# Optimization experiments

Hardware: AMD Instinct MI355X
Metric: run time of the kernel (lower is better)

## Reference

```python
import jax, jax.numpy as jnp
import numpy as np

N = 100000
E = 1600000
D_IN = 128
H1 = 128
H2 = 128
C = 64


def setup_inputs() -> dict:
    key = jax.random.key(0)
    ks = jax.random.split(key, 10)
    x_content = jax.random.normal(ks[0], (N, D_IN), dtype=jnp.float32)
    edge_index = jax.random.randint(ks[1], (2, E), 0, N, dtype=jnp.int64)
    # SAGEConv params: lin_l (applied to aggregated neighbors, has bias),
    # lin_r (applied to root node, no bias). Kaiming-ish scaling.
    def lin(k, fan_in, fan_out):
        return jax.random.normal(k, (fan_in, fan_out), dtype=jnp.float32) / np.sqrt(fan_in)
    return {
        "x_content": x_content,
        "edge_index": edge_index,
        "W1l": lin(ks[2], D_IN, H1),
        "b1": jnp.zeros((H1,), jnp.float32),
        "W1r": lin(ks[3], D_IN, H1),
        "W2l": lin(ks[4], H1, H2),
        "b2": jnp.zeros((H2,), jnp.float32),
        "W2r": lin(ks[5], H1, H2),
        "Wout": lin(ks[6], H2, C),
        "bout": jnp.zeros((C,), jnp.float32),
    }


def _sage_conv(x, src, dst, Wl, b, Wr):
    # mean-aggregate neighbor features (messages flow src -> dst), then
    # out = mean_agg @ Wl + b + x @ Wr  (PyG SAGEConv, aggr='mean')
    msgs = x[src]                                            # [E, d]
    agg = jax.ops.segment_sum(msgs, dst, num_segments=N)     # [N, d]
    deg = jax.ops.segment_sum(jnp.ones((src.shape[0],), x.dtype), dst, num_segments=N)
    mean = agg / jnp.clip(deg, 1.0)[:, None]
    return mean @ Wl + b + x @ Wr


def reference(x_content, edge_index, W1l, b1, W1r, W2l, b2, W2r, Wout, bout):
    src, dst = edge_index[0], edge_index[1]
    # dropout is identity in eval mode (training=False)
    x = jax.nn.relu(_sage_conv(x_content, src, dst, W1l, b1, W1r))
    x = jax.nn.relu(_sage_conv(x, src, dst, W2l, b2, W2r))
    return x @ Wout + bout
```

## Files before the change

### kernel.cpp

```cpp
#include <hip/hip_runtime.h>
#include <hip/hip_fp8.h>

#define DD 128
#define CC 64
#define BKW 512
#define NPB 4096
#define CAP 10240

typedef __attribute__((ext_vector_type(8))) short short8v;
typedef __attribute__((ext_vector_type(4))) float f32x4;
typedef __attribute__((ext_vector_type(2))) float f32x2;

static __device__ inline ushort f2bf_rne(float f) {
    unsigned u = __float_as_uint(f);
    unsigned r = (u + 0x7FFFu + ((u >> 16) & 1u)) >> 16;
    return (ushort)r;
}
static __device__ inline float bf2f(ushort h) {
    return __uint_as_float(((unsigned)h) << 16);
}

__global__ void binit_kernel(int* __restrict__ bcur, int nbuck) {
    int b = blockIdx.x * 256 + threadIdx.x;
    if (b < nbuck) bcur[b] = b * CAP;
}

__global__ __launch_bounds__(256) void binA_kernel(const int* __restrict__ ei,
                                                   int* __restrict__ bcur,
                                                   uint* __restrict__ ebuf, int E) {
    __shared__ int sRun[256];
    __shared__ int sRel[256];
    __shared__ int sBase[256];
    __shared__ uint sPair[NPB];
    __shared__ unsigned char sBkt[NPB];
    __shared__ int sHist[256];
    const int t = threadIdx.x;
    const int e0 = blockIdx.x * NPB;
    const int cntE = min(NPB, E - e0);

    sHist[t] = 0;
    __syncthreads();
    for (int j = t; j < cntE; j += 256) {
        int dst = ei[E + e0 + j];
        atomicAdd(&sHist[dst >> 9], 1);
    }
    __syncthreads();
    int h = sHist[t];
    sRun[t] = h;
    __syncthreads();
    for (int off = 1; off < 256; off <<= 1) {
        int v = 0;
        if (t >= off) v = sRun[t - off];
        __syncthreads();
        if (t >= off) sRun[t] += v;
        __syncthreads();
    }
    int runstart = sRun[t] - h;
    int base = 0;
    if (h > 0) base = atomicAdd(&bcur[t], h);
    sRun[t] = runstart;
    sRel[t] = runstart;
    sBase[t] = base;
    __syncthreads();
    for (int j = t; j < cntE; j += 256) {
        int src = ei[e0 + j];
        int dst = ei[E + e0 + j];
        int b = dst >> 9;
        int slot = atomicAdd(&sRel[b], 1);
        sPair[slot] = (uint)src | ((uint)(dst & 511) << 17);
        sBkt[slot] = (unsigned char)b;
    }
    __syncthreads();
    for (int s = t; s < cntE; s += 256) {
        uint p = sPair[s];
        int b = (int)sBkt[s];
        int gpos = sBase[b] + (s - sRun[b]);
        ebuf[gpos] = p;
    }
}

__global__ __launch_bounds__(256) void binB2_kernel(const uint* __restrict__ ebuf,
                                                    const int* __restrict__ bcur,
                                                    int* __restrict__ offs,
                                                    int* __restrict__ cnt,
                                                    int* __restrict__ csr, int n) {
    __shared__ int sCnt[BKW];
    __shared__ int sOffs[BKW];
    __shared__ int sScan[256];
    const int t = threadIdx.x;
    const int node0 = blockIdx.x * BKW;
    const int start = blockIdx.x * CAP;
    const int end = bcur[blockIdx.x];

    sCnt[t] = 0; sCnt[t + 256] = 0;
    __syncthreads();
    for (int j = start + t; j < end; j += 256) {
        int d = (int)(ebuf[j] >> 17);
        atomicAdd(&sCnt[d], 1);
    }
    __syncthreads();
    int v0 = sCnt[2 * t], v1 = sCnt[2 * t + 1];
    int sum = v0 + v1;
    sScan[t] = sum;
    __syncthreads();
    for (int off = 1; off < 256; off <<= 1) {
        int xv = 0;
        if (t >= off) xv = sScan[t - off];
        __syncthreads();
        if (t >= off) sScan[t] += xv;
        __syncthreads();
    }
    int excl = sScan[t] - sum;
    sOffs[2 * t] = start + excl;
    sOffs[2 * t + 1] = start + excl + v0;
    __syncthreads();
    for (int i = t; i < BKW; i += 256) {
        int node = node0 + i;
        if (node < n) { offs[node] = sOffs[i]; cnt[node] = sCnt[i]; }
    }
    __syncthreads();
    sCnt[t] = 0; sCnt[t + 256] = 0;
    __syncthreads();
    for (int j = start + t; j < end; j += 256) {
        uint p = ebuf[j];
        int d = (int)(p >> 17);
        int r = atomicAdd(&sCnt[d], 1);
        csr[sOffs[d] + r] = (int)(p & 0x1FFFFu);
    }
}

__global__ __launch_bounds__(256) void prep_kernel(
    const float* __restrict__ x, ushort* __restrict__ xh, uint* __restrict__ xq,
    const float* __restrict__ Wl1, const float* __restrict__ Wr1,
    const float* __restrict__ Wl2, const float* __restrict__ Wr2,
    const float* __restrict__ Wout,
    ushort* __restrict__ WTfrag1, ushort* __restrict__ WTfrag2,
    ushort* __restrict__ WoFrag, int nxblk) {
    const int t = threadIdx.x;
    const int bx = blockIdx.x;
    if (bx < nxblk) {
        int i = bx * 256 + t;
        float4 a = ((const float4*)x)[2 * i];
        float4 b = ((const float4*)x)[2 * i + 1];
        float vv[8] = {a.x, a.y, a.z, a.w, b.x, b.y, b.z, b.w};
        ushort r[8];
        uint q[8];
        #pragma unroll
        for (int j = 0; j < 8; ++j) {
            r[j] = f2bf_rne(vv[j]);
            q[j] = (uint)__hip_fp8_e4m3(vv[j]).__x;
        }
        uint4 o;
        o.x = (uint)r[0] | ((uint)r[1] << 16);
        o.y = (uint)r[2] | ((uint)r[3] << 16);
        o.z = (uint)r[4] | ((uint)r[5] << 16);
        o.w = (uint)r[6] | ((uint)r[7] << 16);
        ((uint4*)xh)[i] = o;
        uint2 oq;
        oq.x = q[0] | (q[1] << 8) | (q[2] << 16) | (q[3] << 24);
        oq.y = q[4] | (q[5] << 8) | (q[6] << 16) | (q[7] << 24);
        ((uint2*)xq)[i] = oq;
    } else if (bx < nxblk + 32) {
        int li = bx - nxblk;
        int layer = li >> 4;
        int idx = (li & 15) * 256 + t;
        const float* Wl = layer ? Wl2 : Wl1;
        const float* Wr = layer ? Wr2 : Wr1;
        ushort* dst = (layer ? WTfrag2 : WTfrag1) + (size_t)idx * 8;
        int lane = idx & 63, tt = (idx >> 6) & 7, s = idx >> 9;
        int col = tt * 16 + (lane & 15);
        int k0 = s * 32 + (lane >> 4) * 8;
        #pragma unroll
        for (int j = 0; j < 8; ++j) {
            int k = k0 + j;
            float v = (k < DD) ? Wl[k * DD + col] : Wr[(k - DD) * DD + col];
            dst[j] = f2bf_rne(v);
        }
    } else {
        int idx = (bx - nxblk - 32) * 256 + t;
        ushort* dst = WoFrag + (size_t)idx * 8;
        int lane = idx & 63, tt = (idx >> 6) & 3, kc = idx >> 8;
        int col = tt * 16 + (lane & 15);
        int k0 = kc * 32 + (lane >> 4) * 8;
        #pragma unroll
        for (int j = 0; j < 8; ++j) {
            dst[j] = f2bf_rne(Wout[(k0 + j) * CC + col]);
        }
    }
}

__global__ __launch_bounds__(256) void csr_agg8_kernel(
    const uint* __restrict__ xq, const int* __restrict__ offs,
    const int* __restrict__ cnt, const int* __restrict__ csr,
    ushort* __restrict__ meanH, int n) {
    int node = blockIdx.x * 4 + (threadIdx.x >> 6);
    if (node >= n) return;
    const int lane = threadIdx.x & 63;
    const int sub = lane >> 4;
    const int li = lane & 15;
    const int start = offs[node];
    const int c = cnt[node];
    f32x2 a[4], aa[4];
    #pragma unroll
    for (int k = 0; k < 4; ++k) { a[k] = (f32x2){0.f, 0.f}; aa[k] = (f32x2){0.f, 0.f}; }
    #define ACC8(A, U) { \
        A[0] += __builtin_amdgcn_cvt_pk_f32_fp8(U.x, false); \
        A[1] += __builtin_amdgcn_cvt_pk_f32_fp8(U.x, true);  \
        A[2] += __builtin_amdgcn_cvt_pk_f32_fp8(U.y, false); \
        A[3] += __builtin_amdgcn_cvt_pk_f32_fp8(U.y, true);  }
    const int c16 = c & ~15;
    int j = 0;
    if (c16 > 0) {
        int s0 = csr[start + sub];
        int s1 = csr[start + 4 + sub];
        int s2 = csr[start + 8 + sub];
        int s3 = csr[start + 12 + sub];
        for (; j < c16; j += 16) {
            int t0 = 0, t1 = 0, t2 = 0, t3 = 0;
            if (j + 16 < c16) {
                t0 = csr[start + j + 16 + sub];
                t1 = csr[start + j + 20 + sub];
                t2 = csr[start + j + 24 + sub];
                t3 = csr[start + j + 28 + sub];
            }
            uint2 u0 = *(const uint2*)((const uchar*)xq + (size_t)s0 * DD + li * 8);
            uint2 u1 = *(const uint2*)((const uchar*)xq + (size_t)s1 * DD + li * 8);
            uint2 u2 = *(const uint2*)((const uchar*)xq + (size_t)s2 * DD + li * 8);
            uint2 u3 = *(const uint2*)((const uchar*)xq + (size_t)s3 * DD + li * 8);
            ACC8(a, u0); ACC8(a, u1); ACC8(aa, u2); ACC8(aa, u3);
            s0 = t0; s1 = t1; s2 = t2; s3 = t3;
        }
    }
    if (c - j >= 8) {
        int s0 = csr[start + j + sub];
        int s1 = csr[start + j + 4 + sub];
        uint2 u0 = *(const uint2*)((const uchar*)xq + (size_t)s0 * DD + li * 8);
        uint2 u1 = *(const uint2*)((const uchar*)xq + (size_t)s1 * DD + li * 8);
        ACC8(a, u0); ACC8(aa, u1);
        j += 8;
    }
    if (c - j >= 4) {
        int s = csr[start + j + sub];
        uint2 u = *(const uint2*)((const uchar*)xq + (size_t)s * DD + li * 8);
        ACC8(a, u);
        j += 4;
    }
    if (j + sub < c) {
        int s = csr[start + j + sub];
        uint2 u = *(const uint2*)((const uchar*)xq + (size_t)s * DD + li * 8);
        ACC8(aa, u);
    }
    #undef ACC8
    float res[8];
    #pragma unroll
    for (int k = 0; k < 4; ++k) {
        f32x2 v = a[k] + aa[k];
        float e0 = v.x; e0 += __shfl_xor(e0, 16); e0 += __shfl_xor(e0, 32);
        float e1 = v.y; e1 += __shfl_xor(e1, 16); e1 += __shfl_xor(e1, 32);
        res[2 * k] = e0; res[2 * k + 1] = e1;
    }
    if (sub == 0) {
        float inv = 1.0f / fmaxf((float)c, 1.0f);
        short8v o;
        #pragma unroll
        for (int k = 0; k < 8; ++k) o[k] = (short)f2bf_rne(res[k] * inv);
        *(short8v*)(meanH + (size_t)node * DD + li * 8) = o;
    }
}

template <bool PROJ>
__global__ __launch_bounds__(256) void layer_mfma_kernel(
    const ushort* __restrict__ meanH, const ushort* __restrict__ rootH,
    const ushort* __restrict__ WTfrag, const float* __restrict__ bias,
    ushort* __restrict__ outH, uchar* __restrict__ outQ,
    const ushort* __restrict__ WoFrag, const float* __restrict__ bout,
    float* __restrict__ outF, int n, int ntiles) {
    __shared__ ushort sW[PROJ ? 1 : 4][16][40];
    __shared__ __align__(16) uchar sQ[PROJ ? 1 : 4][16][48];
    __shared__ ushort sH[PROJ ? 2 : 1][16][136];
    const int tid = threadIdx.x;
    const int w = tid >> 6;
    const int l = tid & 63;
    const int lrow16 = l & 15;
    const int kb = (l >> 4) * 8;
    const int lcol = l & 15;
    const int lrow0 = (l >> 4) * 4;

    short8v breg[8][2];
    #pragma unroll
    for (int s = 0; s < 8; ++s) {
        #pragma unroll
        for (int t = 0; t < 2; ++t) {
            breg[s][t] = *(const short8v*)(WTfrag + (size_t)s * 4096 +
                                           (w * 2 + t) * 512 + l * 8);
        }
    }
    float bias_r[2];
    #pragma unroll
    for (int t = 0; t < 2; ++t) bias_r[t] = bias[w * 32 + t * 16 + lcol];

    int pp = 0;
    for (int tile = blockIdx.x; tile < ntiles; tile += gridDim.x, pp ^= 1) {
        const int row0 = tile * 16;
        const int arowg = min(row0 + lrow16, n - 1);
        const ushort* Am = meanH + (size_t)arowg * DD;
        const ushort* Ar = rootH + (size_t)arowg * DD;
        short8v ap[8];
        #pragma unroll
        for (int s = 0; s < 8; ++s) {
            ap[s] = (s < 4) ? *(const short8v*)(Am + s * 32 + kb)
                            : *(const short8v*)(Ar + (s - 4) * 32 + kb);
        }
        f32x4 acc[2];
        acc[0] = (f32x4){0.f, 0.f, 0.f, 0.f};
        acc[1] = (f32x4){0.f, 0.f, 0.f, 0.f};
        #pragma unroll
        for (int s = 0; s < 8; ++s) {
            acc[0] = __builtin_amdgcn_mfma_f32_16x16x32_bf16(ap[s], breg[s][0],
                                                             acc[0], 0, 0, 0);
            acc[1] = __builtin_amdgcn_mfma_f32_16x16x32_bf16(ap[s], breg[s][1],
                                                             acc[1], 0, 0, 0);
        }

        if (!PROJ) {
            #pragma unroll
            for (int t = 0; t < 2; ++t) {
                #pragma unroll
                for (int r = 0; r < 4; ++r) {
                    float o = fmaxf(acc[t][r] + bias_r[t], 0.f);
                    sW[w][lrow0 + r][t * 16 + lcol] = f2bf_rne(o);
                    sQ[w][lrow0 + r][t * 16 + lcol] = __hip_fp8_e4m3(o).__x;
                }
            }
            {
                int row = l >> 2, seg = l & 3;
                int grow = row0 + row;
                if (grow < n)
                    *(uint4*)(outH + (size_t)grow * DD + w * 32 + seg * 8) =
                        *(const uint4*)&sW[w][row][seg * 8];
            }
            if (l < 32) {
                int row = l >> 1, seg = l & 1;
                int grow = row0 + row;
                if (grow < n)
                    *(uint4*)(outQ + (size_t)grow * DD + w * 32 + seg * 16) =
                        *(const uint4*)&sQ[w][row][seg * 16];
            }
        } else {
            #pragma unroll
            for (int t = 0; t < 2; ++t) {
                #pragma unroll
                for (int r = 0; r < 4; ++r) {
                    sH[pp][lrow0 + r][w * 32 + t * 16 + lcol] =
                        f2bf_rne(fmaxf(acc[t][r] + bias_r[t], 0.f));
                }
            }
            __syncthreads();
            f32x4 po = (f32x4){0.f, 0.f, 0.f, 0.f};
            #pragma unroll
            for (int kc = 0; kc < 4; ++kc) {
                short8v ah = *(const short8v*)&sH[pp][lrow16][kc * 32 + kb];
                short8v bh = *(const short8v*)(WoFrag + (size_t)kc * 2048 +
                                               w * 512 + l * 8);
                po = __builtin_amdgcn_mfma_f32_16x16x32_bf16(ah, bh, po, 0, 0, 0);
            }
            const int col = w * 16 + lcol;
            const float b = bout[col];
            #pragma unroll
            for (int r = 0; r < 4; ++r) {
                int grow = row0 + lrow0 + r;
                if (grow < n) outF[(size_t)grow * CC + col] = po[r] + b;
            }
        }
    }
}

extern "C" void kernel_launch(void* const* d_in, const int* in_sizes, int n_in,
                              void* d_out, int out_size, void* d_ws, size_t ws_size,
                              hipStream_t stream) {
    const float* x    = (const float*)d_in[0];
    const int*   ei   = (const int*)d_in[1];
    const float* W1l  = (const float*)d_in[2];
    const float* b1   = (const float*)d_in[3];
    const float* W1r  = (const float*)d_in[4];
    const float* W2l  = (const float*)d_in[5];
    const float* b2   = (const float*)d_in[6];
    const float* W2r  = (const float*)d_in[7];
    const float* Wout = (const float*)d_in[8];
    const float* bout = (const float*)d_in[9];
    float* out = (float*)d_out;
    const int n = in_sizes[0] / DD;
    const int E = in_sizes[1] / 2;
    const size_t NP = (size_t)n * DD;

    const int NBUCK = (n + BKW - 1) / BKW;

    int* offs  = (int*)d_ws;
    int* cnt   = offs + 100352;
    int* bcur  = cnt + 100352;
    int* csr   = bcur + 256;
    uint* ebuf = (uint*)(csr + NBUCK * CAP);
    uint* xq   = ebuf;
    ushort* xh = (ushort*)((uchar*)xq + NP);
    ushort* meanH = xh + NP;
    ushort* h1h = meanH + NP;
    ushort* WTfrag1 = h1h + NP;
    ushort* WTfrag2 = WTfrag1 + 32768;
    ushort* WoFrag  = WTfrag2 + 32768;
    uchar* h1q = (uchar*)(WoFrag + 8192);

    binit_kernel<<<1, 256, 0, stream>>>(bcur, NBUCK);
    binA_kernel<<<(E + NPB - 1) / NPB, 256, 0, stream>>>(ei, bcur, ebuf, E);
    binB2_kernel<<<NBUCK, 256, 0, stream>>>(ebuf, bcur, offs, cnt, csr, n);

    const int nxblk = (int)(NP / 8 / 256);
    prep_kernel<<<nxblk + 36, 256, 0, stream>>>(x, xh, xq, W1l, W1r, W2l, W2r,
                                                Wout, WTfrag1, WTfrag2, WoFrag, nxblk);

    const int ntiles = (n + 15) / 16;
    const int lgrid = 1024;
    const int ablk = (n + 3) / 4;

    csr_agg8_kernel<<<ablk, 256, 0, stream>>>(xq, offs, cnt, csr, meanH, n);
    layer_mfma_kernel<false><<<lgrid, 256, 0, stream>>>(
        meanH, xh, WTfrag1, b1, h1h, h1q,
        (const ushort*)nullptr, (const float*)nullptr, (float*)nullptr, n, ntiles);

    csr_agg8_kernel<<<ablk, 256, 0, stream>>>((const uint*)h1q, offs, cnt, csr, meanH, n);
    layer_mfma_kernel<true><<<lgrid, 256, 0, stream>>>(
        meanH, h1h, WTfrag2, b2, (ushort*)nullptr, (uchar*)nullptr,
        WoFrag, bout, out, n, ntiles);
}
```

Baseline: 206.0 us.

## Fuse CSR mean aggregation into persistent MFMA layer kernel via shared memory

Each persistent block now gathers and averages the FP8 neighbor features for its 16-row tile, one node per wave per iteration, and writes the bf16 means into a double-buffered shared-memory tile. The MFMA reads the means from that tile instead of from a global meanH buffer. This drops two kernel launches and the global write and re-read of the mean matrix, and the grid grows from 1024 to 1536 blocks. In exchange, the irregular gather now shares occupancy with the large MFMA register footprint, and a barrier per tile may serialise gather latency with compute.

```diff
diff --git a/kernel.cpp b/kernel.cpp
--- a/kernel.cpp
+++ b/kernel.cpp
@@ -189,98 +189,24 @@
     }
 }
 
-__global__ __launch_bounds__(256) void csr_agg8_kernel(
-    const uint* __restrict__ xq, const int* __restrict__ offs,
-    const int* __restrict__ cnt, const int* __restrict__ csr,
-    ushort* __restrict__ meanH, int n) {
-    int node = blockIdx.x * 4 + (threadIdx.x >> 6);
-    if (node >= n) return;
-    const int lane = threadIdx.x & 63;
-    const int sub = lane >> 4;
-    const int li = lane & 15;
-    const int start = offs[node];
-    const int c = cnt[node];
-    f32x2 a[4], aa[4];
-    #pragma unroll
-    for (int k = 0; k < 4; ++k) { a[k] = (f32x2){0.f, 0.f}; aa[k] = (f32x2){0.f, 0.f}; }
-    #define ACC8(A, U) { \
-        A[0] += __builtin_amdgcn_cvt_pk_f32_fp8(U.x, false); \
-        A[1] += __builtin_amdgcn_cvt_pk_f32_fp8(U.x, true);  \
-        A[2] += __builtin_amdgcn_cvt_pk_f32_fp8(U.y, false); \
-        A[3] += __builtin_amdgcn_cvt_pk_f32_fp8(U.y, true);  }
-    const int c16 = c & ~15;
-    int j = 0;
-    if (c16 > 0) {
-        int s0 = csr[start + sub];
-        int s1 = csr[start + 4 + sub];
-        int s2 = csr[start + 8 + sub];
-        int s3 = csr[start + 12 + sub];
-        for (; j < c16; j += 16) {
-            int t0 = 0, t1 = 0, t2 = 0, t3 = 0;
-            if (j + 16 < c16) {
-                t0 = csr[start + j + 16 + sub];
-                t1 = csr[start + j + 20 + sub];
-                t2 = csr[start + j + 24 + sub];
-                t3 = csr[start + j + 28 + sub];
-            }
-            uint2 u0 = *(const uint2*)((const uchar*)xq + (size_t)s0 * DD + li * 8);
-            uint2 u1 = *(const uint2*)((const uchar*)xq + (size_t)s1 * DD + li * 8);
-            uint2 u2 = *(const uint2*)((const uchar*)xq + (size_t)s2 * DD + li * 8);
-            uint2 u3 = *(const uint2*)((const uchar*)xq + (size_t)s3 * DD + li * 8);
-            ACC8(a, u0); ACC8(a, u1); ACC8(aa, u2); ACC8(aa, u3);
-            s0 = t0; s1 = t1; s2 = t2; s3 = t3;
-        }
-    }
-    if (c - j >= 8) {
-        int s0 = csr[start + j + sub];
-        int s1 = csr[start + j + 4 + sub];
-        uint2 u0 = *(const uint2*)((const uchar*)xq + (size_t)s0 * DD + li * 8);
-        uint2 u1 = *(const uint2*)((const uchar*)xq + (size_t)s1 * DD + li * 8);
-        ACC8(a, u0); ACC8(aa, u1);
-        j += 8;
-    }
-    if (c - j >= 4) {
-        int s = csr[start + j + sub];
-        uint2 u = *(const uint2*)((const uchar*)xq + (size_t)s * DD + li * 8);
-        ACC8(a, u);
-        j += 4;
-    }
-    if (j + sub < c) {
-        int s = csr[start + j + sub];
-        uint2 u = *(const uint2*)((const uchar*)xq + (size_t)s * DD + li * 8);
-        ACC8(aa, u);
-    }
-    #undef ACC8
-    float res[8];
-    #pragma unroll
-    for (int k = 0; k < 4; ++k) {
-        f32x2 v = a[k] + aa[k];
-        float e0 = v.x; e0 += __shfl_xor(e0, 16); e0 += __shfl_xor(e0, 32);
-        float e1 = v.y; e1 += __shfl_xor(e1, 16); e1 += __shfl_xor(e1, 32);
-        res[2 * k] = e0; res[2 * k + 1] = e1;
-    }
-    if (sub == 0) {
-        float inv = 1.0f / fmaxf((float)c, 1.0f);
-        short8v o;
-        #pragma unroll
-        for (int k = 0; k < 8; ++k) o[k] = (short)f2bf_rne(res[k] * inv);
-        *(short8v*)(meanH + (size_t)node * DD + li * 8) = o;
-    }
-}
-
 template <bool PROJ>
-__global__ __launch_bounds__(256) void layer_mfma_kernel(
-    const ushort* __restrict__ meanH, const ushort* __restrict__ rootH,
+__global__ __launch_bounds__(256) void fused_layer_kernel(
+    const uint* __restrict__ gq, const ushort* __restrict__ rootH,
+    const int* __restrict__ offs, const int* __restrict__ cnt,
+    const int* __restrict__ csr,
     const ushort* __restrict__ WTfrag, const float* __restrict__ bias,
     ushort* __restrict__ outH, uchar* __restrict__ outQ,
     const ushort* __restrict__ WoFrag, const float* __restrict__ bout,
     float* __restrict__ outF, int n, int ntiles) {
+    __shared__ ushort sA[2][16][136];
     __shared__ ushort sW[PROJ ? 1 : 4][16][40];
     __shared__ __align__(16) uchar sQ[PROJ ? 1 : 4][16][48];
     __shared__ ushort sH[PROJ ? 2 : 1][16][136];
     const int tid = threadIdx.x;
     const int w = tid >> 6;
     const int l = tid & 63;
+    const int sub = l >> 4;
+    const int li = l & 15;
     const int lrow16 = l & 15;
     const int kb = (l >> 4) * 8;
     const int lcol = l & 15;
@@ -302,13 +228,88 @@
     int pp = 0;
     for (int tile = blockIdx.x; tile < ntiles; tile += gridDim.x, pp ^= 1) {
         const int row0 = tile * 16;
+
+        for (int nd = 0; nd < 4; ++nd) {
+            const int nodec = min(row0 + w * 4 + nd, n - 1);
+            const int start = offs[nodec];
+            const int c = cnt[nodec];
+            f32x2 a[4], aa[4];
+            #pragma unroll
+            for (int k = 0; k < 4; ++k) {
+                a[k] = (f32x2){0.f, 0.f}; aa[k] = (f32x2){0.f, 0.f};
+            }
+            #define ACC8(A, U) { \
+                A[0] += __builtin_amdgcn_cvt_pk_f32_fp8(U.x, false); \
+                A[1] += __builtin_amdgcn_cvt_pk_f32_fp8(U.x, true);  \
+                A[2] += __builtin_amdgcn_cvt_pk_f32_fp8(U.y, false); \
+                A[3] += __builtin_amdgcn_cvt_pk_f32_fp8(U.y, true);  }
+            const int c16 = c & ~15;
+            int j = 0;
+            if (c16 > 0) {
+                int s0 = csr[start + sub];
+                int s1 = csr[start + 4 + sub];
+                int s2 = csr[start + 8 + sub];
+                int s3 = csr[start + 12 + sub];
+                for (; j < c16; j += 16) {
+                    int t0 = 0, t1 = 0, t2 = 0, t3 = 0;
+                    if (j + 16 < c16) {
+                        t0 = csr[start + j + 16 + sub];
+                        t1 = csr[start + j + 20 + sub];
+                        t2 = csr[start + j + 24 + sub];
+                        t3 = csr[start + j + 28 + sub];
+                    }
+                    uint2 u0 = *(const uint2*)((const uchar*)gq + (size_t)s0 * DD + li * 8);
+                    uint2 u1 = *(const uint2*)((const uchar*)gq + (size_t)s1 * DD + li * 8);
+                    uint2 u2 = *(const uint2*)((const uchar*)gq + (size_t)s2 * DD + li * 8);
+                    uint2 u3 = *(const uint2*)((const uchar*)gq + (size_t)s3 * DD + li * 8);
+                    ACC8(a, u0); ACC8(a, u1); ACC8(aa, u2); ACC8(aa, u3);
+                    s0 = t0; s1 = t1; s2 = t2; s3 = t3;
+                }
+            }
+            if (c - j >= 8) {
+                int s0 = csr[start + j + sub];
+                int s1 = csr[start + j + 4 + sub];
+                uint2 u0 = *(const uint2*)((const uchar*)gq + (size_t)s0 * DD + li * 8);
+                uint2 u1 = *(const uint2*)((const uchar*)gq + (size_t)s1 * DD + li * 8);
+                ACC8(a, u0); ACC8(aa, u1);
+                j += 8;
+            }
+            if (c - j >= 4) {
+                int s = csr[start + j + sub];
+                uint2 u = *(const uint2*)((const uchar*)gq + (size_t)s * DD + li * 8);
+                ACC8(a, u);
+                j += 4;
+            }
+            if (j + sub < c) {
+                int s = csr[start + j + sub];
+                uint2 u = *(const uint2*)((const uchar*)gq + (size_t)s * DD + li * 8);
+                ACC8(aa, u);
+            }
+            #undef ACC8
+            float res[8];
+            #pragma unroll
+            for (int k = 0; k < 4; ++k) {
+                f32x2 v = a[k] + aa[k];
+                float e0 = v.x; e0 += __shfl_xor(e0, 16); e0 += __shfl_xor(e0, 32);
+                float e1 = v.y; e1 += __shfl_xor(e1, 16); e1 += __shfl_xor(e1, 32);
+                res[2 * k] = e0; res[2 * k + 1] = e1;
+            }
+            if (sub == 0) {
+                float inv = 1.0f / fmaxf((float)c, 1.0f);
+                short8v o;
+                #pragma unroll
+                for (int k = 0; k < 8; ++k) o[k] = (short)f2bf_rne(res[k] * inv);
+                *(short8v*)&sA[pp][w * 4 + nd][li * 8] = o;
+            }
+        }
+        __syncthreads();
+
         const int arowg = min(row0 + lrow16, n - 1);
-        const ushort* Am = meanH + (size_t)arowg * DD;
         const ushort* Ar = rootH + (size_t)arowg * DD;
         short8v ap[8];
         #pragma unroll
         for (int s = 0; s < 8; ++s) {
-            ap[s] = (s < 4) ? *(const short8v*)(Am + s * 32 + kb)
+            ap[s] = (s < 4) ? *(const short8v*)&sA[pp][lrow16][s * 32 + kb]
                             : *(const short8v*)(Ar + (s - 4) * 32 + kb);
         }
         f32x4 acc[2];
@@ -402,8 +403,7 @@
     uint* ebuf = (uint*)(csr + NBUCK * CAP);
     uint* xq   = ebuf;
     ushort* xh = (ushort*)((uchar*)xq + NP);
-    ushort* meanH = xh + NP;
-    ushort* h1h = meanH + NP;
+    ushort* h1h = xh + NP;
     ushort* WTfrag1 = h1h + NP;
     ushort* WTfrag2 = WTfrag1 + 32768;
     ushort* WoFrag  = WTfrag2 + 32768;
@@ -418,16 +418,14 @@
                                                 Wout, WTfrag1, WTfrag2, WoFrag, nxblk);
 
     const int ntiles = (n + 15) / 16;
-    const int lgrid = 1024;
-    const int ablk = (n + 3) / 4;
-
-    csr_agg8_kernel<<<ablk, 256, 0, stream>>>(xq, offs, cnt, csr, meanH, n);
-    layer_mfma_kernel<false><<<lgrid, 256, 0, stream>>>(
-        meanH, xh, WTfrag1, b1, h1h, h1q,
+    const int lgrid = 1536;
+
+    fused_layer_kernel<false><<<lgrid, 256, 0, stream>>>(
+        xq, xh, offs, cnt, csr, WTfrag1, b1, h1h, h1q,
         (const ushort*)nullptr, (const float*)nullptr, (float*)nullptr, n, ntiles);
 
-    csr_agg8_kernel<<<ablk, 256, 0, stream>>>((const uint*)h1q, offs, cnt, csr, meanH, n);
-    layer_mfma_kernel<true><<<lgrid, 256, 0, stream>>>(
-        meanH, h1h, WTfrag2, b2, (ushort*)nullptr, (uchar*)nullptr,
+    fused_layer_kernel<true><<<lgrid, 256, 0, stream>>>(
+        (const uint*)h1q, h1h, offs, cnt, csr, WTfrag2, b2,
+        (ushort*)nullptr, (uchar*)nullptr,
         WoFrag, bout, out, n, ntiles);
 }
```

New measurement: 298.6 us. 1.45x slower.
